# Kernel tuning notes

Measured on AMD Instinct MI355X. Metric: run time of the kernel, lower is better.

## Reference

```python
import jax, jax.numpy as jnp
import numpy as np

B, N, K = 4, 250_000, 32
W_FG, W_INST, W_SMOOTH, W_SEED = 1.0, 1.0, 10.0, 10.0


def setup_inputs() -> dict:
    key = jax.random.key(0)
    k1, k2, k3, k4, k5 = jax.random.split(key, 5)
    return {
        "offsets": jax.random.normal(k1, (B, N, 3), jnp.float32),
        "coords": jax.random.normal(k2, (B, N, 3), jnp.float32),
        # small sigma scale so exp(10*sigma_k) stays in a sane range
        "sigmas": jax.random.normal(k3, (B, N, 3), jnp.float32) * 0.05,
        "seeds": jax.random.normal(k4, (B, N), jnp.float32),
        # instance ids in [-1, K); -1 = background
        "instances": jax.random.randint(k5, (B, N), 0, K + 1, jnp.int32) - 1,
    }


def _lovasz_hinge(logits, labels):
    # logits, labels: (B, K, N); vectorized lovasz_hinge_flat per (b, k)
    signs = 2.0 * labels - 1.0
    errors = 1.0 - logits * signs
    order = jnp.argsort(-errors, axis=-1)              # descending sort
    errors_sorted = jnp.take_along_axis(errors, order, axis=-1)
    gt_sorted = jnp.take_along_axis(labels, order, axis=-1)
    gts = jnp.sum(gt_sorted, axis=-1, keepdims=True)
    intersection = gts - jnp.cumsum(gt_sorted, axis=-1)
    union = gts + jnp.cumsum(1.0 - gt_sorted, axis=-1)
    jaccard = 1.0 - intersection / union
    grad = jnp.concatenate([jaccard[..., :1], jaccard[..., 1:] - jaccard[..., :-1]], axis=-1)
    return jnp.sum(jax.nn.relu(errors_sorted) * grad, axis=-1)  # (B, K)


def reference(offsets, coords, sigmas, seeds, instances):
    sg = jax.lax.stop_gradient
    emb = jnp.tanh(offsets) + coords                    # (B, N, 3) spatial embeddings
    seed = jax.nn.sigmoid(seeds)                        # (B, N)

    masks = (instances[:, :, None] == jnp.arange(K)[None, None, :]).astype(jnp.float32)  # (B, N, K)
    counts = jnp.sum(masks, axis=1)                     # (B, K)
    validf = (counts > 0).astype(jnp.float32)
    cnt = jnp.maximum(counts, 1.0)

    # per-instance masked means
    center = jnp.einsum('bnk,bnd->bkd', masks, emb) / cnt[..., None]     # (B, K, 3)
    sigma_k = jnp.einsum('bnk,bnd->bkd', masks, sigmas) / cnt[..., None]  # (B, K, 3)

    # smooth loss: mean over masked (n_k, 3) of (sigma - stop_grad(sigma_k))^2
    sk = sg(sigma_k)
    dev2 = (jnp.einsum('bnk,bnd->bk', masks, sigmas ** 2)
            - 2.0 * jnp.einsum('bnk,bnd,bkd->bk', masks, sigmas, sk)
            + counts * jnp.sum(sk ** 2, axis=-1))
    smooth_k = dev2 / (cnt * 3.0)                       # (B, K)

    s_e = jnp.exp(sigma_k * 10.0)                       # (B, K, 3)
    # quad[b,k,n] = sum_d s_e * (emb - center)^2, expanded to avoid (B,K,N,3)
    quad = (jnp.einsum('bkd,bnd->bkn', s_e, emb ** 2)
            - 2.0 * jnp.einsum('bkd,bnd->bkn', s_e * center, emb)
            + jnp.sum(s_e * center ** 2, axis=-1)[:, :, None])
    probs = jnp.exp(-quad)                              # (B, K, N)
    logits = 2.0 * probs - 1.0

    labels = jnp.transpose(masks, (0, 2, 1))            # (B, K, N)
    lov = _lovasz_hinge(logits, labels)                 # (B, K)

    obj = jnp.maximum(jnp.sum(validf, axis=-1), 1.0)    # (B,)
    instance_loss = jnp.sum(lov * validf, axis=-1) / obj
    smooth_loss = jnp.sum(smooth_k * validf, axis=-1) / obj

    bg = (instances == -1).astype(jnp.float32)
    seed_bg = jnp.sum(bg * seed ** 2, axis=-1)          # (B,)
    seed_fg = W_FG * jnp.sum(labels * (seed[:, None, :] - sg(probs)) ** 2, axis=(-1, -2))
    seed_loss = (seed_bg + seed_fg) / float(N)

    loss = jnp.mean(W_INST * instance_loss + W_SMOOTH * smooth_loss + W_SEED * seed_loss)
    return loss + jnp.sum(offsets) * 0.0
```

## Files before the change

kernel.cpp:

```cpp
#include <hip/hip_runtime.h>
#include <hip/hip_fp16.h>
#include <math.h>

#define B_ 4
#define N_ 250000
#define K_ 32
#define NB 4096
#define NB2 2048
#define KG 2
#define HCH 16
#define S2 16
#define SC 4
#define SLOT_SHIFT 13


__device__ __forceinline__ uint32_t pack_h2(float a, float b) {
  __half2 h = __floats2half2_rn(a, b);
  return *(reinterpret_cast<uint32_t*>(&h));
}
__device__ __forceinline__ float2 unpack_h2(uint32_t u) {
  __half2 h = *(reinterpret_cast<__half2*>(&u));
  return __half22float2(h);
}

__device__ __forceinline__ float quad_qc(float ex, float ey, float ez,
                                         float sex, float sey, float sez,
                                         float tx, float ty, float tz, float A) {
  float q = fmaf(ex, fmaf(sex, ex, -tx),
            fmaf(ey, fmaf(sey, ey, -ty),
            fmaf(ez, fmaf(sez, ez, -tz), A)));
  return fmaxf(q, 0.f);
}

__device__ __forceinline__ float fast_rcp(float x) { return __builtin_amdgcn_rcpf(x); }
__device__ __forceinline__ float fast_tanh(float x) {
  return 1.f - 2.f * fast_rcp(__expf(2.f * x) + 1.f);
}
__device__ __forceinline__ float fast_sigmoid(float x) {
  return fast_rcp(1.f + __expf(-x));
}

__global__ __launch_bounds__(256) void k_emb(
    const float* __restrict__ off, const float* __restrict__ crd,
    const float* __restrict__ seed, const int* __restrict__ inst,
    float* __restrict__ seed_bg, uint2* __restrict__ emb2,
    uint32_t* __restrict__ cursor, uint32_t* __restrict__ list)
{
  __shared__ uint32_t lcnt[K_], lbase[K_];
  __shared__ float red[4];
  const int b = blockIdx.y;
  const int tid = threadIdx.x;
  if (tid < K_) lcnt[tid] = 0;
  __syncthreads();

  const int n0 = blockIdx.x * 1024 + tid * 4;
  int kv[4];
  const bool valid = (n0 < N_);
  float sbg = 0.f;

  if (valid) {
    const int idx = b * N_ + n0;
    const float4* o4 = (const float4*)&off[(size_t)idx * 3];
    const float4* c4 = (const float4*)&crd[(size_t)idx * 3];
    float4 o0 = o4[0], o1 = o4[1], o2 = o4[2];
    float4 c0 = c4[0], c1 = c4[1], c2 = c4[2];
    int4 ki = *(const int4*)&inst[idx];
    kv[0] = ki.x; kv[1] = ki.y; kv[2] = ki.z; kv[3] = ki.w;

    float ex0 = fast_tanh(o0.x) + c0.x, ey0 = fast_tanh(o0.y) + c0.y, ez0 = fast_tanh(o0.z) + c0.z;
    float ex1 = fast_tanh(o0.w) + c0.w, ey1 = fast_tanh(o1.x) + c1.x, ez1 = fast_tanh(o1.y) + c1.y;
    float ex2 = fast_tanh(o1.z) + c1.z, ey2 = fast_tanh(o1.w) + c1.w, ez2 = fast_tanh(o2.x) + c2.x;
    float ex3 = fast_tanh(o2.y) + c2.y, ey3 = fast_tanh(o2.z) + c2.z, ez3 = fast_tanh(o2.w) + c2.w;
    uint4 w0, w1;
    w0.x = pack_h2(ex0, ey0); w0.y = pack_h2(ez0, 0.f);
    w0.z = pack_h2(ex1, ey1); w0.w = pack_h2(ez1, 0.f);
    w1.x = pack_h2(ex2, ey2); w1.y = pack_h2(ez2, 0.f);
    w1.z = pack_h2(ex3, ey3); w1.w = pack_h2(ez3, 0.f);
    ((uint4*)&emb2[idx])[0] = w0;
    ((uint4*)&emb2[idx])[1] = w1;

#pragma unroll
    for (int j = 0; j < 4; ++j) {
      if (kv[j] >= 0) {
        atomicAdd(&lcnt[kv[j]], 1u);
      } else {
        float s = fast_sigmoid(seed[idx + j]);
        sbg = fmaf(s, s, sbg);
      }
    }
  }
  __syncthreads();
  if (tid < K_) {
    uint32_t c = lcnt[tid];
    lbase[tid] = c ? atomicAdd(&cursor[b * K_ + tid], c) : 0u;
    lcnt[tid] = 0;
  }
  __syncthreads();
  if (valid) {
#pragma unroll
    for (int j = 0; j < 4; ++j) {
      if (kv[j] >= 0) {
        uint32_t r = atomicAdd(&lcnt[kv[j]], 1u);
        list[(uint32_t)((b * K_ + kv[j]) << SLOT_SHIFT) + lbase[kv[j]] + r] =
            (uint32_t)(n0 + j);
      }
    }
  }
  for (int d = 32; d > 0; d >>= 1) sbg += __shfl_down(sbg, d, 64);
  int wid = tid >> 6, lane = tid & 63;
  if (lane == 0) red[wid] = sbg;
  __syncthreads();
  if (tid == 0) atomicAdd(&seed_bg[b], red[0] + red[1] + red[2] + red[3]);
}

__global__ __launch_bounds__(256) void k_segstats(
    const uint2* __restrict__ emb2, const float* __restrict__ sig,
    const uint32_t* __restrict__ list, const uint32_t* __restrict__ cursor,
    float* __restrict__ acc)
{
  __shared__ float red[4 * 8];
  const int seg = blockIdx.x >> 2;
  const int c = blockIdx.x & (SC - 1);
  const int b = seg >> 5;
  const int G = (int)cursor[seg];
  if (G == 0) return;
  const int i0 = (int)((long)G * c / SC);
  const int i1 = (int)((long)G * (c + 1) / SC);
  const int base = b * N_;
  const uint32_t lo = (uint32_t)(seg << SLOT_SHIFT);
  const int tid = threadIdx.x;

  float sex_ = 0.f, sey_ = 0.f, sez_ = 0.f;
  float ssx = 0.f, ssy = 0.f, ssz = 0.f, ss2 = 0.f;
  for (int i = i0 + tid; i < i1; i += 256) {
    int idx = base + (int)list[lo + i];
    uint2 e = emb2[idx];
    float2 xy = unpack_h2(e.x);
    float2 zw = unpack_h2(e.y);
    float sx = sig[(size_t)idx * 3 + 0];
    float sy = sig[(size_t)idx * 3 + 1];
    float sz = sig[(size_t)idx * 3 + 2];
    sex_ += xy.x; sey_ += xy.y; sez_ += zw.x;
    ssx += sx; ssy += sy; ssz += sz;
    ss2 = fmaf(sx, sx, fmaf(sy, sy, fmaf(sz, sz, ss2)));
  }
  for (int d = 32; d > 0; d >>= 1) {
    sex_ += __shfl_down(sex_, d, 64); sey_ += __shfl_down(sey_, d, 64);
    sez_ += __shfl_down(sez_, d, 64); ssx  += __shfl_down(ssx,  d, 64);
    ssy  += __shfl_down(ssy,  d, 64); ssz  += __shfl_down(ssz,  d, 64);
    ss2  += __shfl_down(ss2,  d, 64);
  }
  int wid = tid >> 6, lane = tid & 63;
  if (lane == 0) {
    float* r = &red[wid * 8];
    r[0] = sex_; r[1] = sey_; r[2] = sez_;
    r[3] = ssx;  r[4] = ssy;  r[5] = ssz; r[6] = ss2;
  }
  __syncthreads();
  if (tid == 0) {
    float v[7];
    for (int f = 0; f < 7; ++f)
      v[f] = red[f] + red[8 + f] + red[16 + f] + red[24 + f];
    float* a = &acc[seg * 8];
    atomicAdd(&a[0], (float)(i1 - i0));
    atomicAdd(&a[1], v[0]); atomicAdd(&a[2], v[1]); atomicAdd(&a[3], v[2]);
    atomicAdd(&a[4], v[3]); atomicAdd(&a[5], v[4]); atomicAdd(&a[6], v[5]);
    atomicAdd(&a[7], v[6]);
  }
}

__global__ void k_params(const float* __restrict__ acc, float* __restrict__ p05)
{
  int seg = threadIdx.x;
  const float* a = &acc[seg * 8];
  float counts = a[0];
  float cnt = fmaxf(counts, 1.f);
  float inv = 1.f / cnt;
  float cx = a[1] * inv, cy = a[2] * inv, cz = a[3] * inv;
  float skx = a[4] * inv, sky = a[5] * inv, skz = a[6] * inv;
  float sex = expf(10.f * skx), sey = expf(10.f * sky), sez = expf(10.f * skz);
  float dev2 = a[7] - 2.f * (a[4] * skx + a[5] * sky + a[6] * skz)
             + counts * (skx * skx + sky * sky + skz * skz);
  float smooth = dev2 / (cnt * 3.f);
  float A = sex * cx * cx + sey * cy * cy + sez * cz * cz;
  float* o = &p05[seg * 16];
  o[0] = sex; o[1] = sey; o[2] = sez;
  o[3] = 2.f * sex * cx; o[4] = 2.f * sey * cy; o[5] = 2.f * sez * cz;
  o[6] = A; o[7] = counts; o[8] = (counts > 0.f) ? 1.f : 0.f; o[9] = smooth;
}

__global__ __launch_bounds__(512) void k_hist(
    const uint2* __restrict__ emb2, const float* __restrict__ p05,
    uint32_t* __restrict__ hneg_g)
{
  __shared__ uint32_t h[KG * NB];
  const int c = blockIdx.x & (HCH - 1);
  const int kg = blockIdx.x >> 4;
  const int b = blockIdx.y;
  const int seg0 = b * K_ + kg * KG;
  const int tid = threadIdx.x;

  float sexA[KG], seyA[KG], sezA[KG], txA[KG], tyA[KG], tzA[KG], AA[KG];
#pragma unroll
  for (int j = 0; j < KG; ++j) {
    const float* pp = &p05[(seg0 + j) * 16];
    sexA[j] = pp[0]; seyA[j] = pp[1]; sezA[j] = pp[2];
    txA[j] = pp[3]; tyA[j] = pp[4]; tzA[j] = pp[5]; AA[j] = pp[6];
  }
  for (int i = tid; i < KG * NB; i += 512) h[i] = 0;
  __syncthreads();

  const int base = b * N_;
  const int n0 = c * (N_ / HCH);
  const int n1 = n0 + (N_ / HCH);
  for (int n = n0 + tid; n < n1; n += 512) {
    uint2 e = emb2[base + n];
    float2 xy = unpack_h2(e.x);
    float2 zw = unpack_h2(e.y);
#pragma unroll
    for (int j = 0; j < KG; ++j) {
      float qc = quad_qc(xy.x, xy.y, zw.x,
                         sexA[j], seyA[j], sezA[j], txA[j], tyA[j], tzA[j], AA[j]);
      atomicAdd(&h[j * NB + (__float_as_uint(qc) >> 19)], 1u);
    }
  }
  __syncthreads();
#pragma unroll
  for (int j = 0; j < KG; ++j) {
    uint32_t* gn = &hneg_g[(seg0 + j) * NB];
    for (int i = tid; i < NB; i += 512) {
      uint32_t v = h[j * NB + i];
      if (v) atomicAdd(&gn[i], v);
    }
  }
}

__device__ __forceinline__ void scan_excl(uint32_t* h, uint32_t* wsum, int tid)
{
  const int chunk = NB >> 10;
  const int base = tid * chunk;
  uint32_t vals[4];
  uint32_t s = 0;
  for (int i = 0; i < chunk; ++i) { vals[i] = h[base + i]; s += vals[i]; }
  uint32_t x = s;
  int lane = tid & 63;
  for (int d = 1; d < 64; d <<= 1) {
    uint32_t y = (uint32_t)__shfl_up((int)x, d, 64);
    if (lane >= d) x += y;
  }
  int wid = tid >> 6;
  if (lane == 63) wsum[wid] = x;
  __syncthreads();
  if (tid == 0) {
    uint32_t a = 0;
    for (int w = 0; w < 16; ++w) { uint32_t t = wsum[w]; wsum[w] = a; a += t; }
  }
  __syncthreads();
  uint32_t run = wsum[wid] + (x - s);
  for (int i = 0; i < chunk; ++i) { uint32_t t = vals[i]; h[base + i] = run; run += t; }
  __syncthreads();
}

__global__ __launch_bounds__(1024) void k_scanpos(
    const uint2* __restrict__ emb2, const float* __restrict__ seed,
    const float* __restrict__ p05, const uint32_t* __restrict__ list,
    uint32_t* __restrict__ hneg_g, float2* __restrict__ tabN,
    float* __restrict__ lov_out, float* __restrict__ seed_fg)
{
  __shared__ uint32_t hn[NB];
  __shared__ uint32_t hp[NB];
  __shared__ uint32_t wsum[16];
  __shared__ float red[32];
  const int seg = blockIdx.x;
  const int b = seg >> 5;
  const float* pp = &p05[seg * 16];
  const float Gf = pp[7];
  if (Gf <= 0.f) return;
  const float sex = pp[0], sey = pp[1], sez = pp[2];
  const float tx = pp[3], ty = pp[4], tz = pp[5], A = pp[6];
  const int tid = threadIdx.x;
  const int base = b * N_;
  const int G = (int)Gf;
  const uint32_t lo = (uint32_t)(seg << SLOT_SHIFT);
  const float Nnegf = (float)N_ - Gf;

  uint32_t* gn = &hneg_g[seg * NB];
  for (int i = tid; i < NB; i += 1024) { hn[i] = gn[i]; hp[i] = 0; }
  __syncthreads();

  for (int i = tid; i < G; i += 1024) {
    int n = (int)list[lo + i];
    uint2 e = emb2[base + n];
    float2 xy = unpack_h2(e.x);
    float2 zw = unpack_h2(e.y);
    float qc = quad_qc(xy.x, xy.y, zw.x, sex, sey, sez, tx, ty, tz, A);
    atomicAdd(&hn[__float_as_uint(qc) >> 19], 0xFFFFFFFFu);
    float p = __expf(-qc);
    float qs = -__logf(1.f - p);
    atomicAdd(&hp[__float_as_uint(qs) >> 19], 1u);
  }
  __syncthreads();
  scan_excl(hn, wsum, tid);
  scan_excl(hp, wsum, tid);

  float2* tN = &tabN[(size_t)seg * NB2];
  for (int bkt = tid; bkt < NB2; bkt += 1024) {
    float R  = (float)hn[2 * bkt];
    float nn = (bkt < NB2 - 1) ? (float)hn[2 * bkt + 2] : Nnegf;
    float m  = nn - R;
    float pb = (float)hp[2 * bkt];
    float pn = (bkt < NB2 - 1) ? (float)hp[2 * bkt + 2] : Gf;
    float gr = Gf + R;
    float psi2 = 2.f / (gr * (gr + m));
    float u = psi2 * (Gf - pb);
    float v = psi2 * (pn - pb) * (1.f / 1048576.f);
    tN[bkt] = make_float2(u, v);
  }

  float lov = 0.f, sfg = 0.f;
  for (int i = tid; i < G; i += 1024) {
    int n = (int)list[lo + i];
    uint2 e = emb2[base + n];
    float2 xy = unpack_h2(e.x);
    float2 zw = unpack_h2(e.y);
    float qc = quad_qc(xy.x, xy.y, zw.x, sex, sey, sez, tx, ty, tz, A);
    float p = __expf(-qc);
    float qs = -__logf(1.f - p);
    uint32_t qb = __float_as_uint(qs);
    uint32_t bk = qb >> 19;
    float frac = (float)(qb & 0x7FFFFu) * (1.f / 524288.f);
    float R  = (float)hn[bk];
    float nn = (bk < NB - 1) ? (float)hn[bk + 1] : Nnegf;
    float F = R + frac * (nn - R);
    lov += (2.f - 2.f * p) / (Gf + F);
    float s = fast_sigmoid(seed[base + n]);
    float d = s - p;
    sfg += d * d;
    uint32_t cb = __float_as_uint(qc);
    uint32_t b2 = cb >> 20;
    float fr = (float)(cb & 0xFFFFFu);
    float R2  = (float)hn[2 * b2];
    float nn2 = (b2 < NB2 - 1) ? (float)hn[2 * b2 + 2] : Nnegf;
    float m2  = nn2 - R2;
    float pb2 = (float)hp[2 * b2];
    float pn2 = (b2 < NB2 - 1) ? (float)hp[2 * b2 + 2] : Gf;
    float gr2 = Gf + R2;
    float psi2 = 2.f / (gr2 * (gr2 + m2));
    float u2 = psi2 * (Gf - pb2);
    float v2 = psi2 * (pn2 - pb2) * (1.f / 1048576.f);
    lov -= p * fmaf(-v2, fr, u2);
  }

  for (int d = 32; d > 0; d >>= 1) {
    lov += __shfl_down(lov, d, 64);
    sfg += __shfl_down(sfg, d, 64);
  }
  int wid = tid >> 6, lane = tid & 63;
  if (lane == 0) { red[wid] = lov; red[16 + wid] = sfg; }
  __syncthreads();
  if (tid == 0) {
    float lt = 0.f, st = 0.f;
    for (int w = 0; w < 16; ++w) { lt += red[w]; st += red[16 + w]; }
    atomicAdd(&lov_out[seg], lt);
    atomicAdd(&seed_fg[b], st);
  }
}

__global__ __launch_bounds__(256) void k_pass2neg(
    const uint2* __restrict__ emb2, const float* __restrict__ p05,
    const float2* __restrict__ tabN, float* __restrict__ lov_out)
{
  __shared__ float red[4];
  const int seg = blockIdx.x >> 4;
  const int chunk = blockIdx.x & (S2 - 1);
  const int b = seg >> 5;
  const float* pp = &p05[seg * 16];
  const float Gf = pp[7];
  if (Gf <= 0.f) return;
  const float sex = pp[0], sey = pp[1], sez = pp[2];
  const float tx = pp[3], ty = pp[4], tz = pp[5], A = pp[6];
  const int tid = threadIdx.x;
  const int base = b * N_;
  const int n0 = chunk * (N_ / S2);
  const int nfull = n0 + 15360;
  const int n1 = n0 + (N_ / S2);
  const float2* tN = &tabN[(size_t)seg * NB2];

  float l0 = 0.f, l1 = 0.f, l2 = 0.f, l3 = 0.f;
  for (int s = n0 + tid; s < nfull; s += 1024) {
    uint2 e0 = emb2[base + s];
    uint2 e1 = emb2[base + s + 256];
    uint2 e2 = emb2[base + s + 512];
    uint2 e3 = emb2[base + s + 768];
    float2 a0 = unpack_h2(e0.x), b0 = unpack_h2(e0.y);
    float2 a1 = unpack_h2(e1.x), b1 = unpack_h2(e1.y);
    float2 a2 = unpack_h2(e2.x), b2 = unpack_h2(e2.y);
    float2 a3 = unpack_h2(e3.x), b3 = unpack_h2(e3.y);
    float q0 = quad_qc(a0.x, a0.y, b0.x, sex, sey, sez, tx, ty, tz, A);
    float q1 = quad_qc(a1.x, a1.y, b1.x, sex, sey, sez, tx, ty, tz, A);
    float q2 = quad_qc(a2.x, a2.y, b2.x, sex, sey, sez, tx, ty, tz, A);
    float q3 = quad_qc(a3.x, a3.y, b3.x, sex, sey, sez, tx, ty, tz, A);
    uint32_t c0 = __float_as_uint(q0), c1 = __float_as_uint(q1);
    uint32_t c2 = __float_as_uint(q2), c3 = __float_as_uint(q3);
    float2 t0 = tN[c0 >> 20];
    float2 t1 = tN[c1 >> 20];
    float2 t2 = tN[c2 >> 20];
    float2 t3 = tN[c3 >> 20];
    float p0 = __expf(-q0), p1 = __expf(-q1);
    float p2 = __expf(-q2), p3 = __expf(-q3);
    l0 = fmaf(p0, fmaf(-t0.y, (float)(c0 & 0xFFFFFu), t0.x), l0);
    l1 = fmaf(p1, fmaf(-t1.y, (float)(c1 & 0xFFFFFu), t1.x), l1);
    l2 = fmaf(p2, fmaf(-t2.y, (float)(c2 & 0xFFFFFu), t2.x), l2);
    l3 = fmaf(p3, fmaf(-t3.y, (float)(c3 & 0xFFFFFu), t3.x), l3);
  }
  for (int n = nfull + tid; n < n1; n += 256) {
    uint2 e = emb2[base + n];
    float2 xy = unpack_h2(e.x);
    float2 zw = unpack_h2(e.y);
    float qc = quad_qc(xy.x, xy.y, zw.x, sex, sey, sez, tx, ty, tz, A);
    float p = __expf(-qc);
    uint32_t cb = __float_as_uint(qc);
    float2 t = tN[cb >> 20];
    l0 = fmaf(p, fmaf(-t.y, (float)(cb & 0xFFFFFu), t.x), l0);
  }

  float lov = (l0 + l1) + (l2 + l3);
  for (int d = 32; d > 0; d >>= 1) lov += __shfl_down(lov, d, 64);
  int wid = tid >> 6, lane = tid & 63;
  if (lane == 0) red[wid] = lov;
  __syncthreads();
  if (tid == 0) {
    float lt = red[0] + red[1] + red[2] + red[3];
    atomicAdd(&lov_out[seg], lt);
  }
}

__global__ void k_final(const float* __restrict__ p05, const float* __restrict__ lov,
                        const float* __restrict__ seed_bg, const float* __restrict__ seed_fg,
                        float* __restrict__ out)
{
  __shared__ float sv[B_], sl[B_], ss[B_];
  int tid = threadIdx.x;
  if (tid < B_) { sv[tid] = 0.f; sl[tid] = 0.f; ss[tid] = 0.f; }
  __syncthreads();
  int b = tid >> 5;
  float vf = p05[tid * 16 + 8];
  atomicAdd(&sv[b], vf);
  atomicAdd(&sl[b], lov[tid] * vf);
  atomicAdd(&ss[b], p05[tid * 16 + 9] * vf);
  __syncthreads();
  if (tid == 0) {
    float total = 0.f;
    for (int bb = 0; bb < B_; ++bb) {
      float obj = fmaxf(sv[bb], 1.f);
      float seed_l = (seed_bg[bb] + seed_fg[bb]) / (float)N_;
      total += sl[bb] / obj + 10.f * (ss[bb] / obj) + 10.f * seed_l;
    }
    out[0] = total / (float)B_;
  }
}

extern "C" void kernel_launch(void* const* d_in, const int* in_sizes, int n_in,
                              void* d_out, int out_size, void* d_ws, size_t ws_size,
                              hipStream_t stream) {
  const float* off  = (const float*)d_in[0];
  const float* crd  = (const float*)d_in[1];
  const float* sig  = (const float*)d_in[2];
  const float* seed = (const float*)d_in[3];
  const int*   inst = (const int*)d_in[4];

  float* ws      = (float*)d_ws;
  float* acc     = ws;
  float* seed_bg = ws + 1024;
  float* seed_fg = ws + 1028;
  float* lov     = ws + 1032;
  uint32_t* cursor = (uint32_t*)(ws + 1160);
  float* p05     = ws + 2048;
  char* pbase = (char*)d_ws;
  uint2*    emb2   = (uint2*)(pbase + 65536);
  uint32_t* hneg_g = (uint32_t*)(pbase + 65536 + 8388608);
  float2*   tabN   = (float2*)(pbase + 65536 + 8388608 + 2097152);
  uint32_t* list   = (uint32_t*)((char*)tabN + 2097152);

  hipMemsetAsync(d_ws, 0, 8192, stream);
  hipMemsetAsync(hneg_g, 0, 4194304, stream);

  dim3 ge((N_ + 1023) / 1024, B_);
  k_emb<<<ge, 256, 0, stream>>>(off, crd, seed, inst, seed_bg, emb2, cursor, list);
  k_segstats<<<B_ * K_ * SC, 256, 0, stream>>>(emb2, sig, list, cursor, acc);
  k_params<<<1, 128, 0, stream>>>(acc, p05);
  dim3 gh((K_ / KG) * HCH, B_);
  k_hist<<<gh, 512, 0, stream>>>(emb2, p05, hneg_g);
  k_scanpos<<<B_ * K_, 1024, 0, stream>>>(emb2, seed, p05, list, hneg_g, tabN, lov, seed_fg);
  k_pass2neg<<<B_ * K_ * S2, 256, 0, stream>>>(emb2, p05, tabN, lov);
  k_final<<<1, 128, 0, stream>>>(p05, lov, seed_bg, seed_fg, (float*)d_out);
}
```

Measured before the change: 206.6 us.

## Fold memset, params and final reduction into neighbouring kernels to cut launches

Drops the separate 4 MB memset of the negative histogram and instead has k_emb zero the 2 MB region with vector stores. The k_params kernel is removed: every k_hist block derives its segment parameters from the accumulators itself, and chunk 0 writes them to p05 for later kernels. The k_final kernel is merged into k_pass2neg using a last-block-done atomic counter plus a threadfence. This removes three stream operations and their launch gaps, at the cost of redundant parameter math in each k_hist block and a global atomic at the end of each pass2neg block.

```diff
diff --git a/kernel.cpp b/kernel.cpp
--- a/kernel.cpp
+++ b/kernel.cpp
@@ -44,12 +44,19 @@
     const float* __restrict__ off, const float* __restrict__ crd,
     const float* __restrict__ seed, const int* __restrict__ inst,
     float* __restrict__ seed_bg, uint2* __restrict__ emb2,
-    uint32_t* __restrict__ cursor, uint32_t* __restrict__ list)
+    uint32_t* __restrict__ cursor, uint32_t* __restrict__ list,
+    uint32_t* __restrict__ hneg_g)
 {
   __shared__ uint32_t lcnt[K_], lbase[K_];
   __shared__ float red[4];
   const int b = blockIdx.y;
   const int tid = threadIdx.x;
+
+  {
+    int flat = (blockIdx.y * gridDim.x + blockIdx.x) * 256 + tid;
+    if (flat < (2097152 / 16)) ((uint4*)hneg_g)[flat] = make_uint4(0u, 0u, 0u, 0u);
+  }
+
   if (tid < K_) lcnt[tid] = 0;
   __syncthreads();
 
@@ -169,29 +176,9 @@
   }
 }
 
-__global__ void k_params(const float* __restrict__ acc, float* __restrict__ p05)
-{
-  int seg = threadIdx.x;
-  const float* a = &acc[seg * 8];
-  float counts = a[0];
-  float cnt = fmaxf(counts, 1.f);
-  float inv = 1.f / cnt;
-  float cx = a[1] * inv, cy = a[2] * inv, cz = a[3] * inv;
-  float skx = a[4] * inv, sky = a[5] * inv, skz = a[6] * inv;
-  float sex = expf(10.f * skx), sey = expf(10.f * sky), sez = expf(10.f * skz);
-  float dev2 = a[7] - 2.f * (a[4] * skx + a[5] * sky + a[6] * skz)
-             + counts * (skx * skx + sky * sky + skz * skz);
-  float smooth = dev2 / (cnt * 3.f);
-  float A = sex * cx * cx + sey * cy * cy + sez * cz * cz;
-  float* o = &p05[seg * 16];
-  o[0] = sex; o[1] = sey; o[2] = sez;
-  o[3] = 2.f * sex * cx; o[4] = 2.f * sey * cy; o[5] = 2.f * sez * cz;
-  o[6] = A; o[7] = counts; o[8] = (counts > 0.f) ? 1.f : 0.f; o[9] = smooth;
-}
-
 __global__ __launch_bounds__(512) void k_hist(
-    const uint2* __restrict__ emb2, const float* __restrict__ p05,
-    uint32_t* __restrict__ hneg_g)
+    const uint2* __restrict__ emb2, const float* __restrict__ acc,
+    float* __restrict__ p05, uint32_t* __restrict__ hneg_g)
 {
   __shared__ uint32_t h[KG * NB];
   const int c = blockIdx.x & (HCH - 1);
@@ -203,9 +190,24 @@
   float sexA[KG], seyA[KG], sezA[KG], txA[KG], tyA[KG], tzA[KG], AA[KG];
 #pragma unroll
   for (int j = 0; j < KG; ++j) {
-    const float* pp = &p05[(seg0 + j) * 16];
-    sexA[j] = pp[0]; seyA[j] = pp[1]; sezA[j] = pp[2];
-    txA[j] = pp[3]; tyA[j] = pp[4]; tzA[j] = pp[5]; AA[j] = pp[6];
+    const float* a = &acc[(seg0 + j) * 8];
+    float counts = a[0];
+    float cnt = fmaxf(counts, 1.f);
+    float inv = 1.f / cnt;
+    float cx = a[1] * inv, cy = a[2] * inv, cz = a[3] * inv;
+    float skx = a[4] * inv, sky = a[5] * inv, skz = a[6] * inv;
+    sexA[j] = expf(10.f * skx); seyA[j] = expf(10.f * sky); sezA[j] = expf(10.f * skz);
+    txA[j] = 2.f * sexA[j] * cx; tyA[j] = 2.f * seyA[j] * cy; tzA[j] = 2.f * sezA[j] * cz;
+    AA[j] = sexA[j] * cx * cx + seyA[j] * cy * cy + sezA[j] * cz * cz;
+    if (c == 0 && tid == 0) {
+      float dev2 = a[7] - 2.f * (a[4] * skx + a[5] * sky + a[6] * skz)
+                 + counts * (skx * skx + sky * sky + skz * skz);
+      float* o = &p05[(seg0 + j) * 16];
+      o[0] = sexA[j]; o[1] = seyA[j]; o[2] = sezA[j];
+      o[3] = txA[j]; o[4] = tyA[j]; o[5] = tzA[j];
+      o[6] = AA[j]; o[7] = counts;
+      o[8] = (counts > 0.f) ? 1.f : 0.f; o[9] = dev2 / (cnt * 3.f);
+    }
   }
   for (int i = tid; i < KG * NB; i += 512) h[i] = 0;
   __syncthreads();
@@ -368,95 +370,105 @@
 
 __global__ __launch_bounds__(256) void k_pass2neg(
     const uint2* __restrict__ emb2, const float* __restrict__ p05,
-    const float2* __restrict__ tabN, float* __restrict__ lov_out)
+    const float2* __restrict__ tabN, float* __restrict__ lov_out,
+    const float* __restrict__ seed_bg, const float* __restrict__ seed_fg,
+    uint32_t* __restrict__ done, float* __restrict__ out)
 {
   __shared__ float red[4];
+  __shared__ uint32_t slast;
+  __shared__ float sv[B_], sl[B_], ss[B_];
   const int seg = blockIdx.x >> 4;
   const int chunk = blockIdx.x & (S2 - 1);
   const int b = seg >> 5;
   const float* pp = &p05[seg * 16];
   const float Gf = pp[7];
-  if (Gf <= 0.f) return;
-  const float sex = pp[0], sey = pp[1], sez = pp[2];
-  const float tx = pp[3], ty = pp[4], tz = pp[5], A = pp[6];
   const int tid = threadIdx.x;
-  const int base = b * N_;
-  const int n0 = chunk * (N_ / S2);
-  const int nfull = n0 + 15360;
-  const int n1 = n0 + (N_ / S2);
-  const float2* tN = &tabN[(size_t)seg * NB2];
-
-  float l0 = 0.f, l1 = 0.f, l2 = 0.f, l3 = 0.f;
-  for (int s = n0 + tid; s < nfull; s += 1024) {
-    uint2 e0 = emb2[base + s];
-    uint2 e1 = emb2[base + s + 256];
-    uint2 e2 = emb2[base + s + 512];
-    uint2 e3 = emb2[base + s + 768];
-    float2 a0 = unpack_h2(e0.x), b0 = unpack_h2(e0.y);
-    float2 a1 = unpack_h2(e1.x), b1 = unpack_h2(e1.y);
-    float2 a2 = unpack_h2(e2.x), b2 = unpack_h2(e2.y);
-    float2 a3 = unpack_h2(e3.x), b3 = unpack_h2(e3.y);
-    float q0 = quad_qc(a0.x, a0.y, b0.x, sex, sey, sez, tx, ty, tz, A);
-    float q1 = quad_qc(a1.x, a1.y, b1.x, sex, sey, sez, tx, ty, tz, A);
-    float q2 = quad_qc(a2.x, a2.y, b2.x, sex, sey, sez, tx, ty, tz, A);
-    float q3 = quad_qc(a3.x, a3.y, b3.x, sex, sey, sez, tx, ty, tz, A);
-    uint32_t c0 = __float_as_uint(q0), c1 = __float_as_uint(q1);
-    uint32_t c2 = __float_as_uint(q2), c3 = __float_as_uint(q3);
-    float2 t0 = tN[c0 >> 20];
-    float2 t1 = tN[c1 >> 20];
-    float2 t2 = tN[c2 >> 20];
-    float2 t3 = tN[c3 >> 20];
-    float p0 = __expf(-q0), p1 = __expf(-q1);
-    float p2 = __expf(-q2), p3 = __expf(-q3);
-    l0 = fmaf(p0, fmaf(-t0.y, (float)(c0 & 0xFFFFFu), t0.x), l0);
-    l1 = fmaf(p1, fmaf(-t1.y, (float)(c1 & 0xFFFFFu), t1.x), l1);
-    l2 = fmaf(p2, fmaf(-t2.y, (float)(c2 & 0xFFFFFu), t2.x), l2);
-    l3 = fmaf(p3, fmaf(-t3.y, (float)(c3 & 0xFFFFFu), t3.x), l3);
-  }
-  for (int n = nfull + tid; n < n1; n += 256) {
-    uint2 e = emb2[base + n];
-    float2 xy = unpack_h2(e.x);
-    float2 zw = unpack_h2(e.y);
-    float qc = quad_qc(xy.x, xy.y, zw.x, sex, sey, sez, tx, ty, tz, A);
-    float p = __expf(-qc);
-    uint32_t cb = __float_as_uint(qc);
-    float2 t = tN[cb >> 20];
-    l0 = fmaf(p, fmaf(-t.y, (float)(cb & 0xFFFFFu), t.x), l0);
-  }
-
-  float lov = (l0 + l1) + (l2 + l3);
-  for (int d = 32; d > 0; d >>= 1) lov += __shfl_down(lov, d, 64);
-  int wid = tid >> 6, lane = tid & 63;
-  if (lane == 0) red[wid] = lov;
-  __syncthreads();
+
+  if (Gf > 0.f) {
+    const float sex = pp[0], sey = pp[1], sez = pp[2];
+    const float tx = pp[3], ty = pp[4], tz = pp[5], A = pp[6];
+    const int base = b * N_;
+    const int n0 = chunk * (N_ / S2);
+    const int nfull = n0 + 15360;
+    const int n1 = n0 + (N_ / S2);
+    const float2* tN = &tabN[(size_t)seg * NB2];
+
+    float l0 = 0.f, l1 = 0.f, l2 = 0.f, l3 = 0.f;
+    for (int s = n0 + tid; s < nfull; s += 1024) {
+      uint2 e0 = emb2[base + s];
+      uint2 e1 = emb2[base + s + 256];
+      uint2 e2 = emb2[base + s + 512];
+      uint2 e3 = emb2[base + s + 768];
+      float2 a0 = unpack_h2(e0.x), b0 = unpack_h2(e0.y);
+      float2 a1 = unpack_h2(e1.x), b1 = unpack_h2(e1.y);
+      float2 a2 = unpack_h2(e2.x), b2 = unpack_h2(e2.y);
+      float2 a3 = unpack_h2(e3.x), b3 = unpack_h2(e3.y);
+      float q0 = quad_qc(a0.x, a0.y, b0.x, sex, sey, sez, tx, ty, tz, A);
+      float q1 = quad_qc(a1.x, a1.y, b1.x, sex, sey, sez, tx, ty, tz, A);
+      float q2 = quad_qc(a2.x, a2.y, b2.x, sex, sey, sez, tx, ty, tz, A);
+      float q3 = quad_qc(a3.x, a3.y, b3.x, sex, sey, sez, tx, ty, tz, A);
+      uint32_t c0 = __float_as_uint(q0), c1 = __float_as_uint(q1);
+      uint32_t c2 = __float_as_uint(q2), c3 = __float_as_uint(q3);
+      float2 t0 = tN[c0 >> 20];
+      float2 t1 = tN[c1 >> 20];
+      float2 t2 = tN[c2 >> 20];
+      float2 t3 = tN[c3 >> 20];
+      float p0 = __expf(-q0), p1 = __expf(-q1);
+      float p2 = __expf(-q2), p3 = __expf(-q3);
+      l0 = fmaf(p0, fmaf(-t0.y, (float)(c0 & 0xFFFFFu), t0.x), l0);
+      l1 = fmaf(p1, fmaf(-t1.y, (float)(c1 & 0xFFFFFu), t1.x), l1);
+      l2 = fmaf(p2, fmaf(-t2.y, (float)(c2 & 0xFFFFFu), t2.x), l2);
+      l3 = fmaf(p3, fmaf(-t3.y, (float)(c3 & 0xFFFFFu), t3.x), l3);
+    }
+    for (int n = nfull + tid; n < n1; n += 256) {
+      uint2 e = emb2[base + n];
+      float2 xy = unpack_h2(e.x);
+      float2 zw = unpack_h2(e.y);
+      float qc = quad_qc(xy.x, xy.y, zw.x, sex, sey, sez, tx, ty, tz, A);
+      float p = __expf(-qc);
+      uint32_t cb = __float_as_uint(qc);
+      float2 t = tN[cb >> 20];
+      l0 = fmaf(p, fmaf(-t.y, (float)(cb & 0xFFFFFu), t.x), l0);
+    }
+
+    float lov = (l0 + l1) + (l2 + l3);
+    for (int d = 32; d > 0; d >>= 1) lov += __shfl_down(lov, d, 64);
+    int wid = tid >> 6, lane = tid & 63;
+    if (lane == 0) red[wid] = lov;
+    __syncthreads();
+    if (tid == 0) {
+      float lt = red[0] + red[1] + red[2] + red[3];
+      atomicAdd(&lov_out[seg], lt);
+    }
+  }
+
   if (tid == 0) {
-    float lt = red[0] + red[1] + red[2] + red[3];
-    atomicAdd(&lov_out[seg], lt);
-  }
-}
-
-__global__ void k_final(const float* __restrict__ p05, const float* __restrict__ lov,
-                        const float* __restrict__ seed_bg, const float* __restrict__ seed_fg,
-                        float* __restrict__ out)
-{
-  __shared__ float sv[B_], sl[B_], ss[B_];
-  int tid = threadIdx.x;
-  if (tid < B_) { sv[tid] = 0.f; sl[tid] = 0.f; ss[tid] = 0.f; }
-  __syncthreads();
-  int b = tid >> 5;
-  float vf = p05[tid * 16 + 8];
-  atomicAdd(&sv[b], vf);
-  atomicAdd(&sl[b], lov[tid] * vf);
-  atomicAdd(&ss[b], p05[tid * 16 + 9] * vf);
-  __syncthreads();
-  if (tid == 0) {
-    float total = 0.f;
-    for (int bb = 0; bb < B_; ++bb) {
-      float obj = fmaxf(sv[bb], 1.f);
-      float seed_l = (seed_bg[bb] + seed_fg[bb]) / (float)N_;
-      total += sl[bb] / obj + 10.f * (ss[bb] / obj) + 10.f * seed_l;
-    }
-    out[0] = total / (float)B_;
+    __threadfence();
+    uint32_t t = atomicAdd(done, 1u);
+    slast = (t == (uint32_t)(gridDim.x - 1)) ? 1u : 0u;
+  }
+  __syncthreads();
+  if (slast) {
+    if (tid < B_) { sv[tid] = 0.f; sl[tid] = 0.f; ss[tid] = 0.f; }
+    __syncthreads();
+    if (tid < B_ * K_) {
+      int bb = tid >> 5;
+      float vf = p05[tid * 16 + 8];
+      float lv = atomicAdd(&lov_out[tid], 0.f);
+      atomicAdd(&sv[bb], vf);
+      atomicAdd(&sl[bb], lv * vf);
+      atomicAdd(&ss[bb], p05[tid * 16 + 9] * vf);
+    }
+    __syncthreads();
+    if (tid == 0) {
+      float total = 0.f;
+      for (int bb = 0; bb < B_; ++bb) {
+        float obj = fmaxf(sv[bb], 1.f);
+        float seed_l = (seed_bg[bb] + seed_fg[bb]) / (float)N_;
+        total += sl[bb] / obj + 10.f * (ss[bb] / obj) + 10.f * seed_l;
+      }
+      out[0] = total / (float)B_;
+    }
   }
 }
 
@@ -475,6 +487,7 @@
   float* seed_fg = ws + 1028;
   float* lov     = ws + 1032;
   uint32_t* cursor = (uint32_t*)(ws + 1160);
+  uint32_t* done   = (uint32_t*)(ws + 1288);
   float* p05     = ws + 2048;
   char* pbase = (char*)d_ws;
   uint2*    emb2   = (uint2*)(pbase + 65536);
@@ -483,15 +496,14 @@
   uint32_t* list   = (uint32_t*)((char*)tabN + 2097152);
 
   hipMemsetAsync(d_ws, 0, 8192, stream);
-  hipMemsetAsync(hneg_g, 0, 4194304, stream);
 
   dim3 ge((N_ + 1023) / 1024, B_);
-  k_emb<<<ge, 256, 0, stream>>>(off, crd, seed, inst, seed_bg, emb2, cursor, list);
+  k_emb<<<ge, 256, 0, stream>>>(off, crd, seed, inst, seed_bg, emb2, cursor, list,
+                                hneg_g);
   k_segstats<<<B_ * K_ * SC, 256, 0, stream>>>(emb2, sig, list, cursor, acc);
-  k_params<<<1, 128, 0, stream>>>(acc, p05);
   dim3 gh((K_ / KG) * HCH, B_);
-  k_hist<<<gh, 512, 0, stream>>>(emb2, p05, hneg_g);
+  k_hist<<<gh, 512, 0, stream>>>(emb2, acc, p05, hneg_g);
   k_scanpos<<<B_ * K_, 1024, 0, stream>>>(emb2, seed, p05, list, hneg_g, tabN, lov, seed_fg);
-  k_pass2neg<<<B_ * K_ * S2, 256, 0, stream>>>(emb2, p05, tabN, lov);
-  k_final<<<1, 128, 0, stream>>>(p05, lov, seed_bg, seed_fg, (float*)d_out);
-}
+  k_pass2neg<<<B_ * K_ * S2, 256, 0, stream>>>(emb2, p05, tabN, lov,
+                                               seed_bg, seed_fg, done, (float*)d_out);
+}
```

Result: slower. 231.0 us (+11.8%).
